# Optimization experiments

Measured on AMD Instinct MI355X. Metric: run time of the kernel, lower is better.

The kernel has to match this reference:

```python
import math
import jax, jax.numpy as jnp
import numpy as np

HEADS = 8
DIM_HEAD = 64
MAX_POS_EMB = 512


def setup_inputs() -> dict:
    key = jax.random.key(0)
    ks = jax.random.split(key, 6)
    dim = 512
    inner = HEADS * DIM_HEAD  # 512
    x = jax.random.normal(ks[0], (16, 3900, dim), jnp.float32)
    wq = jax.random.normal(ks[1], (dim, inner), jnp.float32) * 0.02
    wkv = jax.random.normal(ks[2], (dim, 2 * inner), jnp.float32) * 0.02
    wout_w = jax.random.normal(ks[3], (inner, dim), jnp.float32) * 0.02
    wout_b = jax.random.normal(ks[4], (dim,), jnp.float32) * 0.02
    rel_pos_table = jax.random.normal(ks[5], (2 * MAX_POS_EMB + 1, DIM_HEAD), jnp.float32) * 0.02
    return {"x": x, "wq": wq, "wkv": wkv, "wout_w": wout_w, "wout_b": wout_b,
            "rel_pos_table": rel_pos_table, "context_size": 200}


def reference(x, wq, wkv, wout_w, wout_b, rel_pos_table, context_size):
    bs, n, d = x.shape
    h, dh = HEADS, DIM_HEAD
    c = context_size
    scale = dh ** -0.5
    nb = math.ceil(n / c)
    nr = n % c
    if nr > 0:
        x = jnp.pad(x, ((0, 0), (0, c - nr), (0, 0)))  # [bs, nb*c, d]
    np_tok = nb * c
    q = x @ wq                     # [bs, np, inner]
    kv = x @ wkv                   # [bs, np, 2*inner]
    k, v = jnp.split(kv, 2, axis=-1)
    # [bs, nb, c, h, dh] -> [bs, nb, h, c, dh]
    def to_heads(t):
        return t.reshape(bs, nb, c, h, dh).transpose(0, 1, 3, 2, 4)
    q, k, v = to_heads(q), to_heads(k), to_heads(v)
    dots = jnp.einsum('bmhid,bmhjd->bmhij', q, k) * scale  # [bs, nb, h, c, c]
    # relative position bias (Transformer-XL style within chunk)
    seq = jnp.arange(c)
    dist = jnp.clip(seq[:, None] - seq[None, :], -c, c) + MAX_POS_EMB  # [c, c]
    rel = rel_pos_table[dist]  # [c, c, dh]
    pos_attn = jnp.einsum('bmhcd,crd->bmhcr', q, rel) * scale
    dots = dots + pos_attn
    if nr > 0:
        # last chunk: mask everything except the valid top-left nr x nr block
        mask = jnp.ones((c, c), dtype=bool).at[:nr, :nr].set(False)
        mask_value = -jnp.finfo(dots.dtype).max
        dots = dots.at[:, -1].set(jnp.where(mask, mask_value, dots[:, -1]))
    attn = jax.nn.softmax(dots, axis=-1)
    out = jnp.einsum('bmhij,bmhjd->bmhid', attn, v)  # [bs, nb, h, c, dh]
    out = out.transpose(0, 1, 3, 2, 4).reshape(bs, np_tok, h * dh)
    out = out[:, :n, :] @ wout_w + wout_b  # dropout is identity at eval
    return out
```

## Files before the change

### kernel.cpp

```cpp
#include <hip/hip_runtime.h>
#include <hip/hip_bf16.h>
#include <cstdint>
#include <cstddef>

#define BS 16
#define SEQ 3900
#define DIM 512
#define NHEAD 8
#define DH 64
#define CHUNK 200
#define NB 20
#define NR 100
#define NP 4000
#define MAXPOS 512
#define MD 62400

typedef __attribute__((ext_vector_type(8))) short bf16x8;
typedef __attribute__((ext_vector_type(8))) unsigned short u16x8;
typedef __attribute__((ext_vector_type(4))) float f32x4;
#define MFMA_BF16 __builtin_amdgcn_mfma_f32_16x16x32_bf16

static __device__ __forceinline__ float bf2f(unsigned short u) {
  union { unsigned int i; float f; } v; v.i = ((unsigned int)u) << 16; return v.f;
}
static __device__ __forceinline__ unsigned short f2bf(float f) {
  unsigned int x = __float_as_uint(f);
  unsigned int lsb = (x >> 16) & 1u;
  x += 0x7fffu + lsb;
  return (unsigned short)(x >> 16);
}
static __device__ __forceinline__ unsigned short f2bf_fast(float f) {
  return (unsigned short)((__float_as_uint(f) + 0x8000u) >> 16);
}

static __device__ __forceinline__ const unsigned short* wt_row(
    const unsigned short* base, int n) {
  unsigned ch = (unsigned)n / 100u;
  unsigned rr = (unsigned)n - ch * 100u;
  return base + (size_t)ch * (NP * DIM) + (size_t)SEQ * DIM + (size_t)rr * DIM;
}

__global__ __launch_bounds__(256) void prep_table(
    const float* __restrict__ table, unsigned short* __restrict__ Tb)
{
  int idx = (blockIdx.x * 256 + threadIdx.x) * 4;
  if (idx < 416 * 64) {
    float4 f = *reinterpret_cast<const float4*>(table + (size_t)305 * 64 + idx);
    ushort4 o;
    o.x = f2bf(f.x); o.y = f2bf(f.y); o.z = f2bf(f.z); o.w = f2bf(f.w);
    *reinterpret_cast<ushort4*>(Tb + idx) = o;
  }
}

__global__ __launch_bounds__(256) void wtrans(
    const float* __restrict__ W, int ldn, int n_off,
    unsigned short* __restrict__ base)
{
  __shared__ float ts[64][65];
  const int tid = threadIdx.x;
  const int n0 = blockIdx.x * 64;
  const int k0 = blockIdx.y * 64;
  {
    int kl = tid >> 4;
    int nl = (tid & 15) * 4;
#pragma unroll
    for (int p = 0; p < 4; ++p) {
      float4 f = *reinterpret_cast<const float4*>(
          W + (size_t)(k0 + kl + p * 16) * ldn + n0 + nl);
      ts[kl + p * 16][nl + 0] = f.x;
      ts[kl + p * 16][nl + 1] = f.y;
      ts[kl + p * 16][nl + 2] = f.z;
      ts[kl + p * 16][nl + 3] = f.w;
    }
  }
  __syncthreads();
  {
    int nl = tid >> 2;
    int kof = (tid & 3) * 16;
    int n = n0 + nl + n_off;
    unsigned ch = (unsigned)n / 100u;
    unsigned rr = (unsigned)n - ch * 100u;
    unsigned short* dst = base + (size_t)ch * (NP * DIM) + (size_t)SEQ * DIM
                          + (size_t)rr * DIM + k0 + kof;
    u16x8 o0, o1;
#pragma unroll
    for (int i = 0; i < 8; ++i) o0[i] = f2bf(ts[kof + i][nl]);
#pragma unroll
    for (int i = 0; i < 8; ++i) o1[i] = f2bf(ts[kof + 8 + i][nl]);
    *reinterpret_cast<u16x8*>(dst) = o0;
    *reinterpret_cast<u16x8*>(dst + 8) = o1;
  }
}

__global__ __launch_bounds__(256) void gemm_qkv(
    const float* __restrict__ x, const unsigned short* __restrict__ WtBase,
    unsigned short* __restrict__ Qb, unsigned short* __restrict__ Kb,
    unsigned short* __restrict__ Vb)
{
  __shared__ unsigned short As[2][128 * 40];
  __shared__ unsigned short Bs[2][128 * 40];

  int bid = blockIdx.x;
  bid = (bid & 7) * 732 + (bid >> 3);
  const int bm = bid / 12, bn = bid % 12;
  const int m0 = bm * 128;
  const int n0 = bn * 128;
  const int tid = threadIdx.x;

  const int ar = tid >> 1;
  const int ac = (tid & 1) * 16;
  int arow = m0 + ar; if (arow > MD - 1) arow = MD - 1;
  const float* ap = x + (size_t)arow * DIM + ac;
  const int awoff = ar * 40 + ac;
  const int br = tid >> 1;
  const int bc = (tid & 1) * 16;
  const unsigned short* bp = wt_row(WtBase, n0 + br) + bc;
  const int bwoff = br * 40 + bc;

  const int wv = tid >> 6, ln = tid & 63;
  const int wr = wv >> 1, wc = wv & 1;
  const int lr = ln & 15, lg = ln >> 4;

  f32x4 acc[4][4];
#pragma unroll
  for (int i = 0; i < 4; ++i)
#pragma unroll
    for (int j = 0; j < 4; ++j) acc[i][j] = (f32x4){0.f, 0.f, 0.f, 0.f};

  {
    float4 f0 = *reinterpret_cast<const float4*>(ap);
    float4 f1 = *reinterpret_cast<const float4*>(ap + 4);
    float4 f2 = *reinterpret_cast<const float4*>(ap + 8);
    float4 f3 = *reinterpret_cast<const float4*>(ap + 12);
    u16x8 w0 = *reinterpret_cast<const u16x8*>(bp);
    u16x8 w1 = *reinterpret_cast<const u16x8*>(bp + 8);
    u16x8 a0, a1;
    a0[0]=f2bf_fast(f0.x); a0[1]=f2bf_fast(f0.y); a0[2]=f2bf_fast(f0.z); a0[3]=f2bf_fast(f0.w);
    a0[4]=f2bf_fast(f1.x); a0[5]=f2bf_fast(f1.y); a0[6]=f2bf_fast(f1.z); a0[7]=f2bf_fast(f1.w);
    a1[0]=f2bf_fast(f2.x); a1[1]=f2bf_fast(f2.y); a1[2]=f2bf_fast(f2.z); a1[3]=f2bf_fast(f2.w);
    a1[4]=f2bf_fast(f3.x); a1[5]=f2bf_fast(f3.y); a1[6]=f2bf_fast(f3.z); a1[7]=f2bf_fast(f3.w);
    *reinterpret_cast<u16x8*>(&As[0][awoff]) = a0;
    *reinterpret_cast<u16x8*>(&As[0][awoff + 8]) = a1;
    *reinterpret_cast<u16x8*>(&Bs[0][bwoff]) = w0;
    *reinterpret_cast<u16x8*>(&Bs[0][bwoff + 8]) = w1;
  }
  __syncthreads();

  int p = 0;
  for (int s = 0; s < 16; ++s) {
    float4 f0, f1, f2, f3; u16x8 w0, w1;
    const bool pre = (s < 15);
    if (pre) {
      int k0 = (s + 1) * 32;
      f0 = *reinterpret_cast<const float4*>(ap + k0);
      f1 = *reinterpret_cast<const float4*>(ap + k0 + 4);
      f2 = *reinterpret_cast<const float4*>(ap + k0 + 8);
      f3 = *reinterpret_cast<const float4*>(ap + k0 + 12);
      w0 = *reinterpret_cast<const u16x8*>(bp + k0);
      w1 = *reinterpret_cast<const u16x8*>(bp + k0 + 8);
    }
    const unsigned short* asp = As[p];
    const unsigned short* bsp = Bs[p];
    bf16x8 af[4], bf[4];
#pragma unroll
    for (int mt = 0; mt < 4; ++mt)
      af[mt] = *reinterpret_cast<const bf16x8*>(asp + (wr * 64 + mt * 16 + lr) * 40 + lg * 8);
#pragma unroll
    for (int nt = 0; nt < 4; ++nt)
      bf[nt] = *reinterpret_cast<const bf16x8*>(bsp + (wc * 64 + nt * 16 + lr) * 40 + lg * 8);
#pragma unroll
    for (int mt = 0; mt < 4; ++mt)
#pragma unroll
      for (int nt = 0; nt < 4; ++nt)
        acc[mt][nt] = MFMA_BF16(af[mt], bf[nt], acc[mt][nt], 0, 0, 0);
    if (pre) {
      u16x8 a0, a1;
      a0[0]=f2bf_fast(f0.x); a0[1]=f2bf_fast(f0.y); a0[2]=f2bf_fast(f0.z); a0[3]=f2bf_fast(f0.w);
      a0[4]=f2bf_fast(f1.x); a0[5]=f2bf_fast(f1.y); a0[6]=f2bf_fast(f1.z); a0[7]=f2bf_fast(f1.w);
      a1[0]=f2bf_fast(f2.x); a1[1]=f2bf_fast(f2.y); a1[2]=f2bf_fast(f2.z); a1[3]=f2bf_fast(f2.w);
      a1[4]=f2bf_fast(f3.x); a1[5]=f2bf_fast(f3.y); a1[6]=f2bf_fast(f3.z); a1[7]=f2bf_fast(f3.w);
      unsigned short* dA = As[p ^ 1];
      unsigned short* dB = Bs[p ^ 1];
      *reinterpret_cast<u16x8*>(&dA[awoff]) = a0;
      *reinterpret_cast<u16x8*>(&dA[awoff + 8]) = a1;
      *reinterpret_cast<u16x8*>(&dB[bwoff]) = w0;
      *reinterpret_cast<u16x8*>(&dB[bwoff + 8]) = w1;
    }
    __syncthreads();
    p ^= 1;
  }

  unsigned short* dst; int nbase;
  if (n0 < 512)       { dst = Qb; nbase = 0; }
  else if (n0 < 1024) { dst = Kb; nbase = 512; }
  else                { dst = Vb; nbase = 1024; }
  const int colg0 = n0 + wc * 64 - nbase;
#pragma unroll
  for (int mt = 0; mt < 4; ++mt) {
#pragma unroll
    for (int e = 0; e < 4; ++e) {
      unsigned rd = m0 + wr * 64 + mt * 16 + lg * 4 + e;
      if (rd < MD) {
        unsigned bb = rd / 3900u;
        unsigned tt = rd - bb * 3900u;
        size_t rowoff = ((size_t)bb * NP + tt) * DIM;
#pragma unroll
        for (int nt = 0; nt < 4; ++nt)
          dst[rowoff + colg0 + nt * 16 + lr] = f2bf(acc[mt][nt][e]);
      }
    }
  }
}

__global__ __launch_bounds__(256) void gemm_out(
    const unsigned short* __restrict__ Ob, const unsigned short* __restrict__ WoBase,
    const float* __restrict__ bias, float* __restrict__ out)
{
  __shared__ unsigned short As[2][128 * 40];
  __shared__ unsigned short Bs[2][128 * 40];

  int bid = blockIdx.x;
  bid = (bid & 7) * 244 + (bid >> 3);
  const int bm = bid / 4, bn = bid % 4;
  const int m0 = bm * 128;
  const int n0 = bn * 128;
  const int tid = threadIdx.x;

  const int ar = tid >> 1;
  const int ac = (tid & 1) * 16;
  unsigned arow = m0 + ar; if (arow > MD - 1) arow = MD - 1;
  unsigned abb = arow / 3900u;
  unsigned att = arow - abb * 3900u;
  const unsigned short* ap = Ob + ((size_t)abb * NP + att) * DIM + ac;
  const int awoff = ar * 40 + ac;

  const int br = tid >> 1;
  const int bc = (tid & 1) * 16;
  const unsigned short* bp = wt_row(WoBase, n0 + br) + bc;
  const int bwoff = br * 40 + bc;

  const int wv = tid >> 6, ln = tid & 63;
  const int wr = wv >> 1, wc = wv & 1;
  const int lr = ln & 15, lg = ln >> 4;

  f32x4 acc[4][4];
#pragma unroll
  for (int i = 0; i < 4; ++i)
#pragma unroll
    for (int j = 0; j < 4; ++j) acc[i][j] = (f32x4){0.f, 0.f, 0.f, 0.f};

  {
    u16x8 a0 = *reinterpret_cast<const u16x8*>(ap);
    u16x8 a1 = *reinterpret_cast<const u16x8*>(ap + 8);
    u16x8 w0 = *reinterpret_cast<const u16x8*>(bp);
    u16x8 w1 = *reinterpret_cast<const u16x8*>(bp + 8);
    *reinterpret_cast<u16x8*>(&As[0][awoff]) = a0;
    *reinterpret_cast<u16x8*>(&As[0][awoff + 8]) = a1;
    *reinterpret_cast<u16x8*>(&Bs[0][bwoff]) = w0;
    *reinterpret_cast<u16x8*>(&Bs[0][bwoff + 8]) = w1;
  }
  __syncthreads();

  int p = 0;
  for (int s = 0; s < 16; ++s) {
    u16x8 a0, a1, w0, w1;
    const bool pre = (s < 15);
    if (pre) {
      int k0 = (s + 1) * 32;
      a0 = *reinterpret_cast<const u16x8*>(ap + k0);
      a1 = *reinterpret_cast<const u16x8*>(ap + k0 + 8);
      w0 = *reinterpret_cast<const u16x8*>(bp + k0);
      w1 = *reinterpret_cast<const u16x8*>(bp + k0 + 8);
    }
    const unsigned short* asp = As[p];
    const unsigned short* bsp = Bs[p];
    bf16x8 af[4], bf[4];
#pragma unroll
    for (int mt = 0; mt < 4; ++mt)
      af[mt] = *reinterpret_cast<const bf16x8*>(asp + (wr * 64 + mt * 16 + lr) * 40 + lg * 8);
#pragma unroll
    for (int nt = 0; nt < 4; ++nt)
      bf[nt] = *reinterpret_cast<const bf16x8*>(bsp + (wc * 64 + nt * 16 + lr) * 40 + lg * 8);
#pragma unroll
    for (int mt = 0; mt < 4; ++mt)
#pragma unroll
      for (int nt = 0; nt < 4; ++nt)
        acc[mt][nt] = MFMA_BF16(af[mt], bf[nt], acc[mt][nt], 0, 0, 0);
    if (pre) {
      unsigned short* dA = As[p ^ 1];
      unsigned short* dB = Bs[p ^ 1];
      *reinterpret_cast<u16x8*>(&dA[awoff]) = a0;
      *reinterpret_cast<u16x8*>(&dA[awoff + 8]) = a1;
      *reinterpret_cast<u16x8*>(&dB[bwoff]) = w0;
      *reinterpret_cast<u16x8*>(&dB[bwoff + 8]) = w1;
    }
    __syncthreads();
    p ^= 1;
  }

  float bv[4];
#pragma unroll
  for (int nt = 0; nt < 4; ++nt) bv[nt] = bias[n0 + wc * 64 + nt * 16 + lr];
#pragma unroll
  for (int mt = 0; mt < 4; ++mt) {
#pragma unroll
    for (int e = 0; e < 4; ++e) {
      unsigned rd = m0 + wr * 64 + mt * 16 + lg * 4 + e;
      if (rd < MD) {
#pragma unroll
        for (int nt = 0; nt < 4; ++nt)
          out[(size_t)rd * DIM + n0 + wc * 64 + nt * 16 + lr] = acc[mt][nt][e] + bv[nt];
      }
    }
  }
}

#define KS_U16 12800
#define VT_U16 13568
#define PQ_STR 228
#define PQ_U16 (16*PQ_STR)
#define ATTN_LDS_B ((KS_U16 + VT_U16 + 4*PQ_U16) * 2)

__global__ __launch_bounds__(256) void attn_mfma(
    const unsigned short* __restrict__ Qb, const unsigned short* __restrict__ Kb,
    const unsigned short* __restrict__ Vb, const unsigned short* __restrict__ Tb,
    unsigned short* __restrict__ Ob)
{
  extern __shared__ unsigned short smem[];
  unsigned short* Ks = smem;
  unsigned short* Vt = smem + KS_U16;

  const int tid = threadIdx.x;
  const int bid = blockIdx.x;
  const int h  = bid & 7;
  const int bm = bid >> 3;
  const int m  = bm % NB;
  const int b  = bm / NB;
  const size_t rowbase = (size_t)b * NP + (size_t)m * CHUNK;
  const int lim = (m == NB - 1) ? NR : CHUNK;

  for (int c = tid; c < CHUNK * 8; c += 256) {
    int j = c >> 3, k0 = (c & 7) * 8;
    uint4 kv = *reinterpret_cast<const uint4*>(Kb + (rowbase + j) * DIM + h * DH + k0);
    int byte = (j * 128 + k0 * 2) ^ ((j & 7) << 4);
    *reinterpret_cast<uint4*>(reinterpret_cast<char*>(Ks) + byte) = kv;
    uint4 vv4 = *reinterpret_cast<const uint4*>(Vb + (rowbase + j) * DIM + h * DH + k0);
    const unsigned short* vs = reinterpret_cast<const unsigned short*>(&vv4);
#pragma unroll
    for (int e = 0; e < 8; ++e)
      Vt[(k0 + e) * 212 + j] = vs[e];
  }
  __syncthreads();

  const int wv = tid >> 6, ln = tid & 63;
  const int lr = ln & 15, lg = ln >> 4;
  unsigned short* pq = smem + KS_U16 + VT_U16 + wv * PQ_U16;

  const int nMt = (lim + 15) >> 4;
  for (int mt = wv; mt < nMt; mt += 4) {
    const int i0 = mt << 4;

    const unsigned short* qp = Qb + (rowbase + i0 + lr) * DIM + h * DH + lg * 8;
    bf16x8 qa0 = *reinterpret_cast<const bf16x8*>(qp);
    bf16x8 qa1 = *reinterpret_cast<const bf16x8*>(qp + 32);

#pragma unroll
    for (int ct = 0; ct < 14; ++ct) {
      const unsigned short* tp = Tb + (size_t)(i0 + ct * 16 + lr) * 64 + lg * 8;
      bf16x8 tb0 = *reinterpret_cast<const bf16x8*>(tp);
      bf16x8 tb1 = *reinterpret_cast<const bf16x8*>(tp + 32);
      f32x4 acc = {0.f, 0.f, 0.f, 0.f};
      acc = MFMA_BF16(qa0, tb0, acc, 0, 0, 0);
      acc = MFMA_BF16(qa1, tb1, acc, 0, 0, 0);
#pragma unroll
      for (int e = 0; e < 4; ++e)
        pq[(lg * 4 + e) * PQ_STR + ct * 16 + lr] = f2bf(acc[e]);
    }

    f32x4 s[13];
#pragma unroll
    for (int nt = 0; nt < 13; ++nt) {
      int row = nt * 16 + lr;
      int b0 = (row * 128 + lg * 16) ^ ((row & 7) << 4);
      int b1 = (row * 128 + 64 + lg * 16) ^ ((row & 7) << 4);
      bf16x8 k0 = *reinterpret_cast<const bf16x8*>(reinterpret_cast<char*>(Ks) + b0);
      bf16x8 k1 = *reinterpret_cast<const bf16x8*>(reinterpret_cast<char*>(Ks) + b1);
      f32x4 acc = {0.f, 0.f, 0.f, 0.f};
      acc = MFMA_BF16(qa0, k0, acc, 0, 0, 0);
      acc = MFMA_BF16(qa1, k1, acc, 0, 0, 0);
      s[nt] = acc;
    }

#pragma unroll
    for (int nt = 0; nt < 13; ++nt) {
      int j = nt * 16 + lr;
#pragma unroll
      for (int e = 0; e < 4; ++e) {
        int r = lg * 4 + e;
        float pos = bf2f(pq[r * PQ_STR + (r - j + 207)]);
        float v = (s[nt][e] + pos) * 0.125f;
        s[nt][e] = (j < lim) ? v : -INFINITY;
      }
    }

    float sum[4];
#pragma unroll
    for (int e = 0; e < 4; ++e) {
      float mv = s[0][e];
#pragma unroll
      for (int nt = 1; nt < 13; ++nt) mv = fmaxf(mv, s[nt][e]);
      mv = fmaxf(mv, __shfl_xor(mv, 1));
      mv = fmaxf(mv, __shfl_xor(mv, 2));
      mv = fmaxf(mv, __shfl_xor(mv, 4));
      mv = fmaxf(mv, __shfl_xor(mv, 8));
      float sv = 0.f;
#pragma unroll
      for (int nt = 0; nt < 13; ++nt) {
        float p = __expf(s[nt][e] - mv);
        s[nt][e] = p;
        sv += p;
      }
      sv += __shfl_xor(sv, 1);
      sv += __shfl_xor(sv, 2);
      sv += __shfl_xor(sv, 4);
      sv += __shfl_xor(sv, 8);
      sum[e] = sv;
    }

#pragma unroll
    for (int nt = 0; nt < 13; ++nt)
#pragma unroll
      for (int e = 0; e < 4; ++e)
        pq[(lg * 4 + e) * PQ_STR + nt * 16 + lr] = f2bf(s[nt][e]);

    f32x4 o[4];
#pragma unroll
    for (int nt = 0; nt < 4; ++nt) o[nt] = (f32x4){0.f, 0.f, 0.f, 0.f};
    const ushort4 zz = {0, 0, 0, 0};
#pragma unroll
    for (int ks = 0; ks < 7; ++ks) {
      union __align__(16) { struct { ushort4 lo, hi; } u; bf16x8 v; } pa;
      if (ks < 6 || lg < 2) {
        const char* pap = reinterpret_cast<const char*>(pq) + lr * (PQ_STR * 2) + ks * 64 + lg * 16;
        pa.u.lo = *reinterpret_cast<const ushort4*>(pap);
        pa.u.hi = *reinterpret_cast<const ushort4*>(pap + 8);
      } else {
        pa.u.lo = zz; pa.u.hi = zz;
      }
#pragma unroll
      for (int nt = 0; nt < 4; ++nt) {
        union __align__(16) { struct { ushort4 lo, hi; } u; bf16x8 v; } vb;
        if (ks < 6 || lg == 0) {
          const char* vbp = reinterpret_cast<const char*>(Vt) + (nt * 16 + lr) * 424 + ks * 64 + lg * 16;
          vb.u.lo = *reinterpret_cast<const ushort4*>(vbp);
          vb.u.hi = *reinterpret_cast<const ushort4*>(vbp + 8);
        } else {
          vb.u.lo = zz; vb.u.hi = zz;
        }
        o[nt] = MFMA_BF16(pa.v, vb.v, o[nt], 0, 0, 0);
      }
    }

#pragma unroll
    for (int nt = 0; nt < 4; ++nt)
#pragma unroll
      for (int e = 0; e < 4; ++e) {
        int i = i0 + lg * 4 + e;
        if (i < lim) {
          float val = o[nt][e] / sum[e];
          Ob[(rowbase + i) * DIM + h * DH + nt * 16 + lr] = f2bf(val);
        }
      }
  }
}

extern "C" void kernel_launch(void* const* d_in, const int* in_sizes, int n_in,
                              void* d_out, int out_size, void* d_ws, size_t ws_size,
                              hipStream_t stream) {
  const float* x   = (const float*)d_in[0];
  const float* wq  = (const float*)d_in[1];
  const float* wkv = (const float*)d_in[2];
  const float* wo  = (const float*)d_in[3];
  const float* wb  = (const float*)d_in[4];
  const float* tbl = (const float*)d_in[5];
  float* out = (float*)d_out;

  const size_t elems = (size_t)BS * NP * DIM;
  unsigned short* Qb = (unsigned short*)d_ws;
  unsigned short* Kb = Qb + elems;
  unsigned short* Vb = Kb + elems;
  unsigned short* Ob = Qb;
  unsigned short* Tb = Kb + (size_t)SEQ * DIM;

  hipFuncSetAttribute(reinterpret_cast<const void*>(attn_mfma),
                      hipFuncAttributeMaxDynamicSharedMemorySize, ATTN_LDS_B);

  dim3 blk(256);
  prep_table<<<dim3(26), blk, 0, stream>>>(tbl, Tb);
  wtrans<<<dim3(8, 8),  blk, 0, stream>>>(wq,  512,  0,   Qb);
  wtrans<<<dim3(16, 8), blk, 0, stream>>>(wkv, 1024, 512, Qb);
  wtrans<<<dim3(8, 8),  blk, 0, stream>>>(wo,  512,  0,   Vb);
  gemm_qkv<<<dim3(5856), blk, 0, stream>>>(x, Qb, Qb, Kb, Vb);
  attn_mfma<<<dim3(BS * NB * NHEAD), blk, ATTN_LDS_B, stream>>>(Qb, Kb, Vb, Tb, Ob);
  gemm_out<<<dim3(1952), blk, 0, stream>>>(Ob, Vb, wb, out);
}
```

Measured before the change: 484.5 us.

## Pre-cast x to bf16 and stage GEMM tiles via direct global-to-LDS loads

Adds a separate kernel that converts x to bf16 into the output buffer, used as scratch, so the QKV GEMM reads bf16 instead of converting fp32 in its inner loop. Both GEMMs now stage A and B tiles with global_load_lds (direct global-to-LDS copies) in an MFMA-fragment-ordered LDS layout, removing the register round trip and the padded row layout. This adds an extra pass over x (fp32 read plus bf16 write), and the unpadded fragment layout may change LDS bank behaviour. The rounding also changes from the fast round-half-up to round-to-nearest-even.

Result: slower. 508.2 us (+4.9%).

```diff
diff --git a/kernel.cpp b/kernel.cpp
--- a/kernel.cpp
+++ b/kernel.cpp
@@ -29,8 +29,13 @@
   x += 0x7fffu + lsb;
   return (unsigned short)(x >> 16);
 }
-static __device__ __forceinline__ unsigned short f2bf_fast(float f) {
-  return (unsigned short)((__float_as_uint(f) + 0x8000u) >> 16);
+
+static __device__ __forceinline__ void gload16(const void* g, void* l) {
+  auto gp = reinterpret_cast<const __attribute__((address_space(1))) unsigned int*>(
+      reinterpret_cast<uintptr_t>(g));
+  auto lp = reinterpret_cast<__attribute__((address_space(3))) unsigned int*>(
+      reinterpret_cast<uintptr_t>(l));
+  __builtin_amdgcn_global_load_lds(gp, lp, 16, 0, 0);
 }
 
 static __device__ __forceinline__ const unsigned short* wt_row(
@@ -92,100 +97,80 @@
   }
 }
 
+__global__ __launch_bounds__(256) void cast_x(
+    const float* __restrict__ x, unsigned short* __restrict__ xb)
+{
+  const size_t total = (size_t)MD * DIM;
+  size_t i = ((size_t)blockIdx.x * 256 + threadIdx.x) * 8;
+  const size_t stride = (size_t)gridDim.x * 256 * 8;
+  for (; i < total; i += stride) {
+    float4 f0 = *reinterpret_cast<const float4*>(x + i);
+    float4 f1 = *reinterpret_cast<const float4*>(x + i + 4);
+    u16x8 o;
+    o[0] = f2bf(f0.x); o[1] = f2bf(f0.y); o[2] = f2bf(f0.z); o[3] = f2bf(f0.w);
+    o[4] = f2bf(f1.x); o[5] = f2bf(f1.y); o[6] = f2bf(f1.z); o[7] = f2bf(f1.w);
+    *reinterpret_cast<u16x8*>(xb + i) = o;
+  }
+}
+
 __global__ __launch_bounds__(256) void gemm_qkv(
-    const float* __restrict__ x, const unsigned short* __restrict__ WtBase,
+    const unsigned short* __restrict__ xb, const unsigned short* __restrict__ WtBase,
     unsigned short* __restrict__ Qb, unsigned short* __restrict__ Kb,
     unsigned short* __restrict__ Vb)
 {
-  __shared__ unsigned short As[2][128 * 40];
-  __shared__ unsigned short Bs[2][128 * 40];
+  __shared__ unsigned short As[2][8 * 512];
+  __shared__ unsigned short Bs[2][8 * 512];
 
   int bid = blockIdx.x;
   bid = (bid & 7) * 732 + (bid >> 3);
   const int bm = bid / 12, bn = bid % 12;
-  const int m0 = bm * 128;
-  const int n0 = bn * 128;
+  const int m0 = bm * 128, n0 = bn * 128;
   const int tid = threadIdx.x;
-
-  const int ar = tid >> 1;
-  const int ac = (tid & 1) * 16;
-  int arow = m0 + ar; if (arow > MD - 1) arow = MD - 1;
-  const float* ap = x + (size_t)arow * DIM + ac;
-  const int awoff = ar * 40 + ac;
-  const int br = tid >> 1;
-  const int bc = (tid & 1) * 16;
-  const unsigned short* bp = wt_row(WtBase, n0 + br) + bc;
-  const int bwoff = br * 40 + bc;
-
   const int wv = tid >> 6, ln = tid & 63;
   const int wr = wv >> 1, wc = wv & 1;
   const int lr = ln & 15, lg = ln >> 4;
 
+  const int sl = ln & 15, sk = (ln >> 4) * 8;
+  const int q0 = wv * 2, q1 = q0 + 1;
+  int ar0 = m0 + (q0 >> 2) * 64 + (q0 & 3) * 16 + sl; if (ar0 >= MD) ar0 = MD - 1;
+  int ar1 = m0 + (q1 >> 2) * 64 + (q1 & 3) * 16 + sl; if (ar1 >= MD) ar1 = MD - 1;
+  const unsigned short* aS0 = xb + (size_t)ar0 * DIM + sk;
+  const unsigned short* aS1 = xb + (size_t)ar1 * DIM + sk;
+  const unsigned short* bS0 = wt_row(WtBase, n0 + (q0 >> 2) * 64 + (q0 & 3) * 16 + sl) + sk;
+  const unsigned short* bS1 = wt_row(WtBase, n0 + (q1 >> 2) * 64 + (q1 & 3) * 16 + sl) + sk;
+
   f32x4 acc[4][4];
 #pragma unroll
   for (int i = 0; i < 4; ++i)
 #pragma unroll
     for (int j = 0; j < 4; ++j) acc[i][j] = (f32x4){0.f, 0.f, 0.f, 0.f};
 
-  {
-    float4 f0 = *reinterpret_cast<const float4*>(ap);
-    float4 f1 = *reinterpret_cast<const float4*>(ap + 4);
-    float4 f2 = *reinterpret_cast<const float4*>(ap + 8);
-    float4 f3 = *reinterpret_cast<const float4*>(ap + 12);
-    u16x8 w0 = *reinterpret_cast<const u16x8*>(bp);
-    u16x8 w1 = *reinterpret_cast<const u16x8*>(bp + 8);
-    u16x8 a0, a1;
-    a0[0]=f2bf_fast(f0.x); a0[1]=f2bf_fast(f0.y); a0[2]=f2bf_fast(f0.z); a0[3]=f2bf_fast(f0.w);
-    a0[4]=f2bf_fast(f1.x); a0[5]=f2bf_fast(f1.y); a0[6]=f2bf_fast(f1.z); a0[7]=f2bf_fast(f1.w);
-    a1[0]=f2bf_fast(f2.x); a1[1]=f2bf_fast(f2.y); a1[2]=f2bf_fast(f2.z); a1[3]=f2bf_fast(f2.w);
-    a1[4]=f2bf_fast(f3.x); a1[5]=f2bf_fast(f3.y); a1[6]=f2bf_fast(f3.z); a1[7]=f2bf_fast(f3.w);
-    *reinterpret_cast<u16x8*>(&As[0][awoff]) = a0;
-    *reinterpret_cast<u16x8*>(&As[0][awoff + 8]) = a1;
-    *reinterpret_cast<u16x8*>(&Bs[0][bwoff]) = w0;
-    *reinterpret_cast<u16x8*>(&Bs[0][bwoff + 8]) = w1;
-  }
+#define STG_QKV(buf, koff)                          \
+  gload16(aS0 + (koff), &As[buf][q0 * 512]);        \
+  gload16(aS1 + (koff), &As[buf][q1 * 512]);        \
+  gload16(bS0 + (koff), &Bs[buf][q0 * 512]);        \
+  gload16(bS1 + (koff), &Bs[buf][q1 * 512]);
+
+  STG_QKV(0, 0)
   __syncthreads();
 
   int p = 0;
   for (int s = 0; s < 16; ++s) {
-    float4 f0, f1, f2, f3; u16x8 w0, w1;
-    const bool pre = (s < 15);
-    if (pre) {
-      int k0 = (s + 1) * 32;
-      f0 = *reinterpret_cast<const float4*>(ap + k0);
-      f1 = *reinterpret_cast<const float4*>(ap + k0 + 4);
-      f2 = *reinterpret_cast<const float4*>(ap + k0 + 8);
-      f3 = *reinterpret_cast<const float4*>(ap + k0 + 12);
-      w0 = *reinterpret_cast<const u16x8*>(bp + k0);
-      w1 = *reinterpret_cast<const u16x8*>(bp + k0 + 8);
-    }
+    if (s < 15) { STG_QKV(p ^ 1, (s + 1) * 32) }
     const unsigned short* asp = As[p];
     const unsigned short* bsp = Bs[p];
-    bf16x8 af[4], bf[4];
+    bf16x8 af[4], bfr[4];
 #pragma unroll
     for (int mt = 0; mt < 4; ++mt)
-      af[mt] = *reinterpret_cast<const bf16x8*>(asp + (wr * 64 + mt * 16 + lr) * 40 + lg * 8);
+      af[mt] = *reinterpret_cast<const bf16x8*>(asp + (wr * 4 + mt) * 512 + ln * 8);
 #pragma unroll
     for (int nt = 0; nt < 4; ++nt)
-      bf[nt] = *reinterpret_cast<const bf16x8*>(bsp + (wc * 64 + nt * 16 + lr) * 40 + lg * 8);
+      bfr[nt] = *reinterpret_cast<const bf16x8*>(bsp + (wc * 4 + nt) * 512 + ln * 8);
 #pragma unroll
     for (int mt = 0; mt < 4; ++mt)
 #pragma unroll
       for (int nt = 0; nt < 4; ++nt)
-        acc[mt][nt] = MFMA_BF16(af[mt], bf[nt], acc[mt][nt], 0, 0, 0);
-    if (pre) {
-      u16x8 a0, a1;
-      a0[0]=f2bf_fast(f0.x); a0[1]=f2bf_fast(f0.y); a0[2]=f2bf_fast(f0.z); a0[3]=f2bf_fast(f0.w);
-      a0[4]=f2bf_fast(f1.x); a0[5]=f2bf_fast(f1.y); a0[6]=f2bf_fast(f1.z); a0[7]=f2bf_fast(f1.w);
-      a1[0]=f2bf_fast(f2.x); a1[1]=f2bf_fast(f2.y); a1[2]=f2bf_fast(f2.z); a1[3]=f2bf_fast(f2.w);
-      a1[4]=f2bf_fast(f3.x); a1[5]=f2bf_fast(f3.y); a1[6]=f2bf_fast(f3.z); a1[7]=f2bf_fast(f3.w);
-      unsigned short* dA = As[p ^ 1];
-      unsigned short* dB = Bs[p ^ 1];
-      *reinterpret_cast<u16x8*>(&dA[awoff]) = a0;
-      *reinterpret_cast<u16x8*>(&dA[awoff + 8]) = a1;
-      *reinterpret_cast<u16x8*>(&dB[bwoff]) = w0;
-      *reinterpret_cast<u16x8*>(&dB[bwoff + 8]) = w1;
-    }
+        acc[mt][nt] = MFMA_BF16(af[mt], bfr[nt], acc[mt][nt], 0, 0, 0);
     __syncthreads();
     p ^= 1;
   }
@@ -216,84 +201,61 @@
     const unsigned short* __restrict__ Ob, const unsigned short* __restrict__ WoBase,
     const float* __restrict__ bias, float* __restrict__ out)
 {
-  __shared__ unsigned short As[2][128 * 40];
-  __shared__ unsigned short Bs[2][128 * 40];
+  __shared__ unsigned short As[2][8 * 512];
+  __shared__ unsigned short Bs[2][8 * 512];
 
   int bid = blockIdx.x;
   bid = (bid & 7) * 244 + (bid >> 3);
   const int bm = bid / 4, bn = bid % 4;
-  const int m0 = bm * 128;
-  const int n0 = bn * 128;
+  const int m0 = bm * 128, n0 = bn * 128;
   const int tid = threadIdx.x;
-
-  const int ar = tid >> 1;
-  const int ac = (tid & 1) * 16;
-  unsigned arow = m0 + ar; if (arow > MD - 1) arow = MD - 1;
-  unsigned abb = arow / 3900u;
-  unsigned att = arow - abb * 3900u;
-  const unsigned short* ap = Ob + ((size_t)abb * NP + att) * DIM + ac;
-  const int awoff = ar * 40 + ac;
-
-  const int br = tid >> 1;
-  const int bc = (tid & 1) * 16;
-  const unsigned short* bp = wt_row(WoBase, n0 + br) + bc;
-  const int bwoff = br * 40 + bc;
-
   const int wv = tid >> 6, ln = tid & 63;
   const int wr = wv >> 1, wc = wv & 1;
   const int lr = ln & 15, lg = ln >> 4;
 
+  const int sl = ln & 15, sk = (ln >> 4) * 8;
+  const int q0 = wv * 2, q1 = q0 + 1;
+  unsigned ar0 = m0 + (q0 >> 2) * 64 + (q0 & 3) * 16 + sl; if (ar0 >= MD) ar0 = MD - 1;
+  unsigned ar1 = m0 + (q1 >> 2) * 64 + (q1 & 3) * 16 + sl; if (ar1 >= MD) ar1 = MD - 1;
+  unsigned b0b = ar0 / 3900u, t0 = ar0 - b0b * 3900u;
+  unsigned b1b = ar1 / 3900u, t1 = ar1 - b1b * 3900u;
+  const unsigned short* aS0 = Ob + ((size_t)b0b * NP + t0) * DIM + sk;
+  const unsigned short* aS1 = Ob + ((size_t)b1b * NP + t1) * DIM + sk;
+  const unsigned short* bS0 = wt_row(WoBase, n0 + (q0 >> 2) * 64 + (q0 & 3) * 16 + sl) + sk;
+  const unsigned short* bS1 = wt_row(WoBase, n0 + (q1 >> 2) * 64 + (q1 & 3) * 16 + sl) + sk;
+
   f32x4 acc[4][4];
 #pragma unroll
   for (int i = 0; i < 4; ++i)
 #pragma unroll
     for (int j = 0; j < 4; ++j) acc[i][j] = (f32x4){0.f, 0.f, 0.f, 0.f};
 
-  {
-    u16x8 a0 = *reinterpret_cast<const u16x8*>(ap);
-    u16x8 a1 = *reinterpret_cast<const u16x8*>(ap + 8);
-    u16x8 w0 = *reinterpret_cast<const u16x8*>(bp);
-    u16x8 w1 = *reinterpret_cast<const u16x8*>(bp + 8);
-    *reinterpret_cast<u16x8*>(&As[0][awoff]) = a0;
-    *reinterpret_cast<u16x8*>(&As[0][awoff + 8]) = a1;
-    *reinterpret_cast<u16x8*>(&Bs[0][bwoff]) = w0;
-    *reinterpret_cast<u16x8*>(&Bs[0][bwoff + 8]) = w1;
-  }
+#define STG_OUT(buf, koff)                          \
+  gload16(aS0 + (koff), &As[buf][q0 * 512]);        \
+  gload16(aS1 + (koff), &As[buf][q1 * 512]);        \
+  gload16(bS0 + (koff), &Bs[buf][q0 * 512]);        \
+  gload16(bS1 + (koff), &Bs[buf][q1 * 512]);
+
+  STG_OUT(0, 0)
   __syncthreads();
 
   int p = 0;
   for (int s = 0; s < 16; ++s) {
-    u16x8 a0, a1, w0, w1;
-    const bool pre = (s < 15);
-    if (pre) {
-      int k0 = (s + 1) * 32;
-      a0 = *reinterpret_cast<const u16x8*>(ap + k0);
-      a1 = *reinterpret_cast<const u16x8*>(ap + k0 + 8);
-      w0 = *reinterpret_cast<const u16x8*>(bp + k0);
-      w1 = *reinterpret_cast<const u16x8*>(bp + k0 + 8);
-    }
+    if (s < 15) { STG_OUT(p ^ 1, (s + 1) * 32) }
     const unsigned short* asp = As[p];
     const unsigned short* bsp = Bs[p];
-    bf16x8 af[4], bf[4];
+    bf16x8 af[4], bfr[4];
 #pragma unroll
     for (int mt = 0; mt < 4; ++mt)
-      af[mt] = *reinterpret_cast<const bf16x8*>(asp + (wr * 64 + mt * 16 + lr) * 40 + lg * 8);
+      af[mt] = *reinterpret_cast<const bf16x8*>(asp + (wr * 4 + mt) * 512 + ln * 8);
 #pragma unroll
     for (int nt = 0; nt < 4; ++nt)
-      bf[nt] = *reinterpret_cast<const bf16x8*>(bsp + (wc * 64 + nt * 16 + lr) * 40 + lg * 8);
+      bfr[nt] = *reinterpret_cast<const bf16x8*>(bsp + (wc * 4 + nt) * 512 + ln * 8);
 #pragma unroll
     for (int mt = 0; mt < 4; ++mt)
 #pragma unroll
       for (int nt = 0; nt < 4; ++nt)
-        acc[mt][nt] = MFMA_BF16(af[mt], bf[nt], acc[mt][nt], 0, 0, 0);
-    if (pre) {
-      unsigned short* dA = As[p ^ 1];
-      unsigned short* dB = Bs[p ^ 1];
-      *reinterpret_cast<u16x8*>(&dA[awoff]) = a0;
-      *reinterpret_cast<u16x8*>(&dA[awoff + 8]) = a1;
-      *reinterpret_cast<u16x8*>(&dB[bwoff]) = w0;
-      *reinterpret_cast<u16x8*>(&dB[bwoff + 8]) = w1;
-    }
+        acc[mt][nt] = MFMA_BF16(af[mt], bfr[nt], acc[mt][nt], 0, 0, 0);
     __syncthreads();
     p ^= 1;
   }
@@ -491,6 +453,7 @@
   unsigned short* Vb = Kb + elems;
   unsigned short* Ob = Qb;
   unsigned short* Tb = Kb + (size_t)SEQ * DIM;
+  unsigned short* xb = (unsigned short*)d_out;
 
   hipFuncSetAttribute(reinterpret_cast<const void*>(attn_mfma),
                       hipFuncAttributeMaxDynamicSharedMemorySize, ATTN_LDS_B);
@@ -500,7 +463,8 @@
   wtrans<<<dim3(8, 8),  blk, 0, stream>>>(wq,  512,  0,   Qb);
   wtrans<<<dim3(16, 8), blk, 0, stream>>>(wkv, 1024, 512, Qb);
   wtrans<<<dim3(8, 8),  blk, 0, stream>>>(wo,  512,  0,   Vb);
-  gemm_qkv<<<dim3(5856), blk, 0, stream>>>(x, Qb, Qb, Kb, Vb);
+  cast_x<<<dim3(2048), blk, 0, stream>>>(x, xb);
+  gemm_qkv<<<dim3(5856), blk, 0, stream>>>(xb, Qb, Qb, Kb, Vb);
   attn_mfma<<<dim3(BS * NB * NHEAD), blk, ATTN_LDS_B, stream>>>(Qb, Kb, Vb, Tb, Ob);
   gemm_out<<<dim3(1952), blk, 0, stream>>>(Ob, Vb, wb, out);
 }
```
